# Kernel optimization log

Hardware: AMD Instinct MI355X
Metric: run time of the kernel (lower is better)

The kernel has to match this reference:

```python
import jax, jax.numpy as jnp
import numpy as np

B, Q, D, N = 128, 20, 11, 100000  # batch, produced vectors per sample, feature dim, song DB size
EPS = 1e-8  # torch cosine_similarity eps


def setup_inputs() -> dict:
    key = jax.random.key(0)
    ks = jax.random.split(key, 8)
    x = jax.random.normal(ks[0], (B, 5, 11), dtype=jnp.float32)
    W1 = jax.random.normal(ks[1], (55, 128), dtype=jnp.float32) * 0.1
    b1 = jnp.zeros((128,), dtype=jnp.float32)
    W2 = jax.random.normal(ks[2], (128, 64), dtype=jnp.float32) * 0.1
    b2 = jnp.zeros((64,), dtype=jnp.float32)
    W3 = jax.random.normal(ks[3], (64, Q * D), dtype=jnp.float32) * 0.1
    b3 = jnp.zeros((Q * D,), dtype=jnp.float32)
    songs = jax.random.normal(ks[4], (N, D), dtype=jnp.float32)
    return {"x": x, "W1": W1, "b1": b1, "W2": W2, "b2": b2, "W3": W3, "b3": b3, "songs": songs}


def reference(x, W1, b1, W2, b2, W3, b3, songs):
    # Encoder MLP: Flatten -> Linear -> ReLU -> Linear -> ReLU -> Linear
    h = x.reshape(x.shape[0], -1)                 # [B, 55]
    h = jax.nn.relu(h @ W1 + b1)                  # [B, 128]
    h = jax.nn.relu(h @ W2 + b2)                  # [B, 64]
    produced = (h @ W3 + b3).reshape(-1, Q, D)    # [B, 20, 11]

    # Batched cosine-similarity kNN (k=1 / argmax) against the song DB.
    # torch cosine_similarity: a.b / (max(||a||, eps) * max(||b||, eps))
    p_norm = produced / jnp.maximum(jnp.linalg.norm(produced, axis=-1, keepdims=True), EPS)
    s_norm = songs / jnp.maximum(jnp.linalg.norm(songs, axis=-1, keepdims=True), EPS)
    sim = jnp.einsum('bqd,nd->bqn', p_norm, s_norm)  # [B, Q, N]
    best = jnp.argmax(sim, axis=-1)                  # [B, Q]
    return songs[best]                                # [B, Q, D]
```

## Files before the change

### kernel.cpp

```cpp
#include <hip/hip_runtime.h>
#include <math.h>

#define EPS 1e-8f

constexpr int B_ = 128;
constexpr int Q_ = 20;
constexpr int D_ = 11;
constexpr int N_ = 100000;
constexpr int DP_ = 12;
constexpr int NPAIR = B_ * Q_;
constexpr int NCH = 1000;
constexpr int CS = N_ / NCH;
constexpr int NG = CS / 4;
constexpr int TPB = 128;
constexpr int PPT = 4;
constexpr int REP = NPAIR / (PPT * TPB);
constexpr int CPB = 2;
constexpr int NPB = NCH / CPB;
constexpr int MPAD = (NPB + 7) / 8;
constexpr int SGRID = 8 * MPAD * REP;

typedef __attribute__((ext_vector_type(4))) float f4;

__global__ void prep_kernel(const float* __restrict__ x,
                            const float* __restrict__ W1, const float* __restrict__ b1,
                            const float* __restrict__ W2, const float* __restrict__ b2,
                            const float* __restrict__ W3, const float* __restrict__ b3,
                            const float* __restrict__ songs,
                            float* __restrict__ pnorm, float* __restrict__ snorm,
                            int do_snorm)
{
    const int t = threadIdx.x;
    if (blockIdx.x >= B_) {
        if (!do_snorm) return;
        const int i = (blockIdx.x - B_) * blockDim.x + t;
        if (i >= N_) return;
        float v[DP_]; float ss = 0.0f;
#pragma unroll
        for (int d = 0; d < D_; ++d) { v[d] = songs[(size_t)i * D_ + d]; ss += v[d] * v[d]; }
        float nrm = fmaxf(sqrtf(ss), EPS);
#pragma unroll
        for (int d = 0; d < D_; ++d) v[d] /= nrm;
        v[D_] = 0.0f;
        float4* o = reinterpret_cast<float4*>(snorm + (size_t)i * DP_);
        o[0] = make_float4(v[0], v[1], v[2], v[3]);
        o[1] = make_float4(v[4], v[5], v[6], v[7]);
        o[2] = make_float4(v[8], v[9], v[10], v[11]);
        return;
    }
    __shared__ float xr[55];
    __shared__ float h1[128];
    __shared__ float h2[64];
    __shared__ float prod[220];
    const int b = blockIdx.x;
    if (t < 55) xr[t] = x[b * 55 + t];
    __syncthreads();
    if (t < 128) {
        float s = b1[t];
        for (int k = 0; k < 55; ++k) s += xr[k] * W1[k * 128 + t];
        h1[t] = fmaxf(s, 0.0f);
    }
    __syncthreads();
    if (t < 64) {
        float s = b2[t];
        for (int k = 0; k < 128; ++k) s += h1[k] * W2[k * 64 + t];
        h2[t] = fmaxf(s, 0.0f);
    }
    __syncthreads();
    if (t < 220) {
        float s = b3[t];
        for (int k = 0; k < 64; ++k) s += h2[k] * W3[k * 220 + t];
        prod[t] = s;
    }
    __syncthreads();
    if (t < Q_) {
        float ss = 0.0f;
        for (int d = 0; d < D_; ++d) { float v = prod[t * D_ + d]; ss += v * v; }
        float nrm = fmaxf(sqrtf(ss), EPS);
        float* o = pnorm + (b * Q_ + t) * DP_;
        for (int d = 0; d < D_; ++d) o[d] = prod[t * D_ + d] / nrm;
        o[D_] = 0.0f;
    }
}

__device__ __forceinline__ float dot11v(f4 qa, f4 qb, f4 qc,
                                        float4 a, float4 b, float4 c)
{
    float x = qa.x * a.x;
    x = fmaf(qa.y, a.y, x);
    x = fmaf(qa.z, a.z, x);
    x = fmaf(qa.w, a.w, x);
    x = fmaf(qb.x, b.x, x);
    x = fmaf(qb.y, b.y, x);
    x = fmaf(qb.z, b.z, x);
    x = fmaf(qb.w, b.w, x);
    x = fmaf(qc.x, c.x, x);
    x = fmaf(qc.y, c.y, x);
    x = fmaf(qc.z, c.z, x);
    return x;
}

__device__ __forceinline__ unsigned int fkey(float f)
{
    unsigned int b = __float_as_uint(f);
    return (b & 0x80000000u) ? ~b : (b | 0x80000000u);
}

__device__ __forceinline__ unsigned long long pack_vi(float v, int idx)
{
    return ((unsigned long long)fkey(v) << 32) | (unsigned long long)(0xFFFFFFFFu - (unsigned int)idx);
}

#define QLOAD(P, PTR) \
    asm volatile("global_load_dwordx4 %0, %3, off\n\t" \
                 "global_load_dwordx4 %1, %3, off offset:16\n\t" \
                 "global_load_dwordx4 %2, %3, off offset:32" \
                 : "=&v"(q##P##a), "=&v"(q##P##b), "=&v"(q##P##c) \
                 : "v"(PTR) : "memory")

#define QWAIT() \
    asm volatile("s_waitcnt vmcnt(0)" \
                 : "+v"(qAa), "+v"(qAb), "+v"(qAc), "+v"(qBa), "+v"(qBb), "+v"(qBc), \
                   "+v"(qCa), "+v"(qCb), "+v"(qCc), "+v"(qDa), "+v"(qDb), "+v"(qDc) \
                 :: "memory")

#define PMAXV(P, G) { \
    float d0 = dot11v(q##P##a, q##P##b, q##P##c, s0, s1,  s2);  \
    float d1 = dot11v(q##P##a, q##P##b, q##P##c, s3, s4,  s5);  \
    float d2 = dot11v(q##P##a, q##P##b, q##P##c, s6, s7,  s8);  \
    float d3 = dot11v(q##P##a, q##P##b, q##P##c, s9, s10, s11); \
    float mx = fmaxf(fmaxf(d0, d1), fmaxf(d2, d3)); \
    if (mx > bv##P) { bv##P = mx; gi##P = (G); } \
}

#define GSTEP(L4, G, GOFF) { \
    const float4* vg = (L4) + (G) * 12; \
    float4 s0 = vg[0], s1 = vg[1], s2  = vg[2],  s3  = vg[3],  s4  = vg[4],  s5  = vg[5]; \
    float4 s6 = vg[6], s7 = vg[7], s8  = vg[8],  s9  = vg[9],  s10 = vg[10], s11 = vg[11]; \
    PMAXV(A, (GOFF) + (G)) PMAXV(B, (GOFF) + (G)) PMAXV(C, (GOFF) + (G)) PMAXV(D, (GOFF) + (G)) \
}

#define FINI(P, POFF) { \
    int gsel = gi##P; \
    int cs = (gsel >= NG) ? 1 : 0; \
    int gg = gsel - cs * NG; \
    const float4* vg = reinterpret_cast<const float4*>(lds[cs]) + gg * 12; \
    float4 s0 = vg[0], s1 = vg[1], s2  = vg[2],  s3  = vg[3],  s4  = vg[4],  s5  = vg[5]; \
    float4 s6 = vg[6], s7 = vg[7], s8  = vg[8],  s9  = vg[9],  s10 = vg[10], s11 = vg[11]; \
    float d0 = dot11v(q##P##a, q##P##b, q##P##c, s0, s1,  s2);  \
    float d1 = dot11v(q##P##a, q##P##b, q##P##c, s3, s4,  s5);  \
    float d2 = dot11v(q##P##a, q##P##b, q##P##c, s6, s7,  s8);  \
    float d3 = dot11v(q##P##a, q##P##b, q##P##c, s9, s10, s11); \
    int base = (c0 + cs) * CS + gg * 4; \
    int idx = base; \
    if (d3 == bv##P) idx = base + 3; \
    if (d2 == bv##P) idx = base + 2; \
    if (d1 == bv##P) idx = base + 1; \
    if (d0 == bv##P) idx = base; \
    atomicMax(&res[jb + (POFF) * TPB], pack_vi(bv##P, idx)); \
}

__global__ __launch_bounds__(TPB, 2)
void sim13_kernel(const float* __restrict__ pnorm,
                  const float* __restrict__ snorm,
                  unsigned long long* __restrict__ res)
{
    __shared__ __align__(16) float lds[CPB][CS * DP_];
    const int bid = blockIdx.x;
    const int u = bid & 7;
    const int kk = bid >> 3;
    const int r = kk % REP;
    const int m = kk / REP;
    const int cpair = u + 8 * m;
    if (cpair >= NPB) return;
    const int t = threadIdx.x;
    const int c0 = cpair * CPB;

    const float4* s40 = reinterpret_cast<const float4*>(snorm) + (size_t)c0 * CS * 3;
    const float4* s41 = s40 + CS * 3;
    float4* b0 = reinterpret_cast<float4*>(lds[0]);
    float4* b1 = reinterpret_cast<float4*>(lds[1]);

    b0[t] = s40[t];
    b0[t + TPB] = s40[t + TPB];
    if (t < CS * 3 - 2 * TPB) b0[t + 2 * TPB] = s40[t + 2 * TPB];

    const int jb = r * (PPT * TPB) + t;
    f4 qAa, qAb, qAc, qBa, qBb, qBc, qCa, qCb, qCc, qDa, qDb, qDc;
    {
        const float* qp0 = pnorm + (size_t)(jb + 0 * TPB) * DP_;
        const float* qp1 = pnorm + (size_t)(jb + 1 * TPB) * DP_;
        const float* qp2 = pnorm + (size_t)(jb + 2 * TPB) * DP_;
        const float* qp3 = pnorm + (size_t)(jb + 3 * TPB) * DP_;
        QLOAD(A, qp0);
        QLOAD(B, qp1);
        QLOAD(C, qp2);
        QLOAD(D, qp3);
    }
    QWAIT();

    float4 r0 = s41[t];
    float4 r1 = s41[t + TPB];
    float4 r2 = make_float4(0.f, 0.f, 0.f, 0.f);
    if (t < CS * 3 - 2 * TPB) r2 = s41[t + 2 * TPB];

    __syncthreads();

    float bvA = -1e30f, bvB = -1e30f, bvC = -1e30f, bvD = -1e30f;
    int giA = 0, giB = 0, giC = 0, giD = 0;

    for (int g = 0; g < NG; ++g) {
        GSTEP(b0, g, 0);
    }

    b1[t] = r0;
    b1[t + TPB] = r1;
    if (t < CS * 3 - 2 * TPB) b1[t + 2 * TPB] = r2;
    __syncthreads();

    for (int g = 0; g < NG; ++g) {
        GSTEP(b1, g, NG);
    }

    FINI(A, 0) FINI(B, 1) FINI(C, 2) FINI(D, 3)
}

template<int FNCH>
__global__ void sim6f_kernel(const float* __restrict__ pnorm,
                             const float* __restrict__ songs,
                             unsigned long long* __restrict__ res)
{
    constexpr int FCS = N_ / FNCH;
    const int chunk = blockIdx.x;
    const int j = blockIdx.y * 256 + threadIdx.x;

    float qv[D_];
#pragma unroll
    for (int d = 0; d < D_; ++d) qv[d] = pnorm[j * DP_ + d];

    float bestv = -1e30f;
    int   besti = 0;
    const int base = chunk * FCS;
    for (int i = base; i < base + FCS; ++i) {
        float sv[D_]; float ss = 0.0f;
#pragma unroll
        for (int d = 0; d < D_; ++d) { sv[d] = songs[(size_t)i * D_ + d]; ss += sv[d] * sv[d]; }
        float nrm = fmaxf(sqrtf(ss), EPS);
        float a = qv[0] * (sv[0] / nrm);
#pragma unroll
        for (int d = 1; d < D_; ++d) a = fmaf(qv[d], sv[d] / nrm, a);
        if (a > bestv) { bestv = a; besti = i; }
    }
    atomicMax(&res[j], pack_vi(bestv, besti));
}

__global__ void gather_kernel(const unsigned long long* __restrict__ res,
                              const float* __restrict__ songs, float* __restrict__ out)
{
    const int j = blockIdx.x * blockDim.x + threadIdx.x;
    if (j >= NPAIR) return;
    const unsigned int idx = 0xFFFFFFFFu - (unsigned int)(res[j] & 0xFFFFFFFFull);
#pragma unroll
    for (int d = 0; d < D_; ++d) out[(size_t)j * D_ + d] = songs[(size_t)idx * D_ + d];
}

extern "C" void kernel_launch(void* const* d_in, const int* in_sizes, int n_in,
                              void* d_out, int out_size, void* d_ws, size_t ws_size,
                              hipStream_t stream)
{
    const float* x     = (const float*)d_in[0];
    const float* W1    = (const float*)d_in[1];
    const float* b1    = (const float*)d_in[2];
    const float* W2    = (const float*)d_in[3];
    const float* b2    = (const float*)d_in[4];
    const float* W3    = (const float*)d_in[5];
    const float* b3    = (const float*)d_in[6];
    const float* songs = (const float*)d_in[7];
    float* out = (float*)d_out;

    constexpr size_t PN = (size_t)NPAIR * DP_;
    constexpr size_t SN = (size_t)N_ * DP_;
    float* pnorm = (float*)d_ws;
    constexpr int SNB = (N_ + 255) / 256;

    const size_t need_full = (PN + SN) * sizeof(float) + (size_t)NPAIR * 8 + 64;
    const size_t need_min  = PN * sizeof(float) + (size_t)NPAIR * 8 + 64;

    if (ws_size >= need_full) {
        float* snorm = pnorm + PN;
        unsigned long long* res =
            (unsigned long long*)(((uintptr_t)(snorm + SN) + 7) & ~(uintptr_t)7);
        hipMemsetAsync(res, 0, (size_t)NPAIR * 8, stream);
        prep_kernel<<<B_ + SNB, 256, 0, stream>>>(x, W1, b1, W2, b2, W3, b3, songs,
                                                  pnorm, snorm, 1);
        sim13_kernel<<<SGRID, TPB, 0, stream>>>(pnorm, snorm, res);
        gather_kernel<<<(NPAIR + 255) / 256, 256, 0, stream>>>(res, songs, out);
    } else if (ws_size >= need_min) {
        unsigned long long* res =
            (unsigned long long*)(((uintptr_t)(pnorm + PN) + 7) & ~(uintptr_t)7);
        hipMemsetAsync(res, 0, (size_t)NPAIR * 8, stream);
        prep_kernel<<<B_, 256, 0, stream>>>(x, W1, b1, W2, b2, W3, b3, songs,
                                            pnorm, nullptr, 0);
        constexpr int FNCH = 250;
        sim6f_kernel<FNCH><<<dim3(FNCH, NPAIR / 256), 256, 0, stream>>>(pnorm, songs, res);
        gather_kernel<<<(NPAIR + 255) / 256, 256, 0, stream>>>(res, songs, out);
    }
}
```

Before: 91.69 us.

## Process eight query pairs per thread with 64-thread blocks in similarity kernel

Halves the block size to one wavefront and doubles the query vectors held per thread from four to eight, so each LDS-loaded song group is reused across more dot products. This lowers LDS read traffic per FMA and per-block staging overhead. The cost is higher register pressure from 24 extra query VGPRs plus more best-value trackers, which may reduce occupancy. The launch bound is changed to ask for three blocks per CU.

```diff
diff --git a/kernel.cpp b/kernel.cpp
--- a/kernel.cpp
+++ b/kernel.cpp
@@ -12,8 +12,8 @@
 constexpr int NCH = 1000;
 constexpr int CS = N_ / NCH;
 constexpr int NG = CS / 4;
-constexpr int TPB = 128;
-constexpr int PPT = 4;
+constexpr int TPB = 64;
+constexpr int PPT = 8;
 constexpr int REP = NPAIR / (PPT * TPB);
 constexpr int CPB = 2;
 constexpr int NPB = NCH / CPB;
@@ -121,23 +121,28 @@
 #define QWAIT() \
     asm volatile("s_waitcnt vmcnt(0)" \
                  : "+v"(qAa), "+v"(qAb), "+v"(qAc), "+v"(qBa), "+v"(qBb), "+v"(qBc), \
-                   "+v"(qCa), "+v"(qCb), "+v"(qCc), "+v"(qDa), "+v"(qDb), "+v"(qDc) \
+                   "+v"(qCa), "+v"(qCb), "+v"(qCc), "+v"(qDa), "+v"(qDb), "+v"(qDc), \
+                   "+v"(qEa), "+v"(qEb), "+v"(qEc), "+v"(qFa), "+v"(qFb), "+v"(qFc), \
+                   "+v"(qGa), "+v"(qGb), "+v"(qGc), "+v"(qHa), "+v"(qHb), "+v"(qHc) \
                  :: "memory")
 
-#define PMAXV(P, G) { \
+#define PMAXV(P, GCUR) { \
     float d0 = dot11v(q##P##a, q##P##b, q##P##c, s0, s1,  s2);  \
     float d1 = dot11v(q##P##a, q##P##b, q##P##c, s3, s4,  s5);  \
     float d2 = dot11v(q##P##a, q##P##b, q##P##c, s6, s7,  s8);  \
     float d3 = dot11v(q##P##a, q##P##b, q##P##c, s9, s10, s11); \
     float mx = fmaxf(fmaxf(d0, d1), fmaxf(d2, d3)); \
-    if (mx > bv##P) { bv##P = mx; gi##P = (G); } \
-}
-
-#define GSTEP(L4, G, GOFF) { \
-    const float4* vg = (L4) + (G) * 12; \
+    if (mx > bv##P) { bv##P = mx; gi##P = (GCUR); } \
+}
+
+#define GSTEP(L4, GIDX, GOFF) { \
+    const float4* vg = (L4) + (GIDX) * 12; \
     float4 s0 = vg[0], s1 = vg[1], s2  = vg[2],  s3  = vg[3],  s4  = vg[4],  s5  = vg[5]; \
     float4 s6 = vg[6], s7 = vg[7], s8  = vg[8],  s9  = vg[9],  s10 = vg[10], s11 = vg[11]; \
-    PMAXV(A, (GOFF) + (G)) PMAXV(B, (GOFF) + (G)) PMAXV(C, (GOFF) + (G)) PMAXV(D, (GOFF) + (G)) \
+    PMAXV(A, (GOFF) + (GIDX)) PMAXV(B, (GOFF) + (GIDX)) \
+    PMAXV(C, (GOFF) + (GIDX)) PMAXV(D, (GOFF) + (GIDX)) \
+    PMAXV(E, (GOFF) + (GIDX)) PMAXV(F, (GOFF) + (GIDX)) \
+    PMAXV(G, (GOFF) + (GIDX)) PMAXV(H, (GOFF) + (GIDX)) \
 }
 
 #define FINI(P, POFF) { \
@@ -160,8 +165,8 @@
     atomicMax(&res[jb + (POFF) * TPB], pack_vi(bv##P, idx)); \
 }
 
-__global__ __launch_bounds__(TPB, 2)
-void sim13_kernel(const float* __restrict__ pnorm,
+__global__ __launch_bounds__(TPB, 3)
+void sim14_kernel(const float* __restrict__ pnorm,
                   const float* __restrict__ snorm,
                   unsigned long long* __restrict__ res)
 {
@@ -181,33 +186,39 @@
     float4* b0 = reinterpret_cast<float4*>(lds[0]);
     float4* b1 = reinterpret_cast<float4*>(lds[1]);
 
-    b0[t] = s40[t];
-    b0[t + TPB] = s40[t + TPB];
-    if (t < CS * 3 - 2 * TPB) b0[t + 2 * TPB] = s40[t + 2 * TPB];
+#pragma unroll
+    for (int i = 0; i < 4; ++i) b0[t + i * TPB] = s40[t + i * TPB];
+    if (t < CS * 3 - 4 * TPB) b0[t + 4 * TPB] = s40[t + 4 * TPB];
 
     const int jb = r * (PPT * TPB) + t;
     f4 qAa, qAb, qAc, qBa, qBb, qBc, qCa, qCb, qCc, qDa, qDb, qDc;
+    f4 qEa, qEb, qEc, qFa, qFb, qFc, qGa, qGb, qGc, qHa, qHb, qHc;
     {
-        const float* qp0 = pnorm + (size_t)(jb + 0 * TPB) * DP_;
-        const float* qp1 = pnorm + (size_t)(jb + 1 * TPB) * DP_;
-        const float* qp2 = pnorm + (size_t)(jb + 2 * TPB) * DP_;
-        const float* qp3 = pnorm + (size_t)(jb + 3 * TPB) * DP_;
-        QLOAD(A, qp0);
-        QLOAD(B, qp1);
-        QLOAD(C, qp2);
-        QLOAD(D, qp3);
+        const float* p0 = pnorm + (size_t)(jb + 0 * TPB) * DP_;
+        const float* p1 = pnorm + (size_t)(jb + 1 * TPB) * DP_;
+        const float* p2 = pnorm + (size_t)(jb + 2 * TPB) * DP_;
+        const float* p3 = pnorm + (size_t)(jb + 3 * TPB) * DP_;
+        const float* p4 = pnorm + (size_t)(jb + 4 * TPB) * DP_;
+        const float* p5 = pnorm + (size_t)(jb + 5 * TPB) * DP_;
+        const float* p6 = pnorm + (size_t)(jb + 6 * TPB) * DP_;
+        const float* p7 = pnorm + (size_t)(jb + 7 * TPB) * DP_;
+        QLOAD(A, p0); QLOAD(B, p1); QLOAD(C, p2); QLOAD(D, p3);
+        QLOAD(E, p4); QLOAD(F, p5); QLOAD(G, p6); QLOAD(H, p7);
     }
     QWAIT();
 
     float4 r0 = s41[t];
     float4 r1 = s41[t + TPB];
-    float4 r2 = make_float4(0.f, 0.f, 0.f, 0.f);
-    if (t < CS * 3 - 2 * TPB) r2 = s41[t + 2 * TPB];
+    float4 r2 = s41[t + 2 * TPB];
+    float4 r3 = s41[t + 3 * TPB];
+    float4 r4 = make_float4(0.f, 0.f, 0.f, 0.f);
+    if (t < CS * 3 - 4 * TPB) r4 = s41[t + 4 * TPB];
 
     __syncthreads();
 
     float bvA = -1e30f, bvB = -1e30f, bvC = -1e30f, bvD = -1e30f;
-    int giA = 0, giB = 0, giC = 0, giD = 0;
+    float bvE = -1e30f, bvF = -1e30f, bvG = -1e30f, bvH = -1e30f;
+    int giA = 0, giB = 0, giC = 0, giD = 0, giE = 0, giF = 0, giG = 0, giH = 0;
 
     for (int g = 0; g < NG; ++g) {
         GSTEP(b0, g, 0);
@@ -215,7 +226,9 @@
 
     b1[t] = r0;
     b1[t + TPB] = r1;
-    if (t < CS * 3 - 2 * TPB) b1[t + 2 * TPB] = r2;
+    b1[t + 2 * TPB] = r2;
+    b1[t + 3 * TPB] = r3;
+    if (t < CS * 3 - 4 * TPB) b1[t + 4 * TPB] = r4;
     __syncthreads();
 
     for (int g = 0; g < NG; ++g) {
@@ -223,6 +236,7 @@
     }
 
     FINI(A, 0) FINI(B, 1) FINI(C, 2) FINI(D, 3)
+    FINI(E, 4) FINI(F, 5) FINI(G, 6) FINI(H, 7)
 }
 
 template<int FNCH>
@@ -293,7 +307,7 @@
         hipMemsetAsync(res, 0, (size_t)NPAIR * 8, stream);
         prep_kernel<<<B_ + SNB, 256, 0, stream>>>(x, W1, b1, W2, b2, W3, b3, songs,
                                                   pnorm, snorm, 1);
-        sim13_kernel<<<SGRID, TPB, 0, stream>>>(pnorm, snorm, res);
+        sim14_kernel<<<SGRID, TPB, 0, stream>>>(pnorm, snorm, res);
         gather_kernel<<<(NPAIR + 255) / 256, 256, 0, stream>>>(res, songs, out);
     } else if (ws_size >= need_min) {
         unsigned long long* res =
```

Result: slower. 106.9 us (+16.6%).
